# Performance work log

Measured on AMD Instinct MI355X. Metric: run time of the kernel, lower is better.

The kernel has to match this reference:

```python
import jax, jax.numpy as jnp
import numpy as np

B, R, K, D = 65536, 8, 8, 256


def setup_inputs() -> dict:
    key = jax.random.key(0)
    ks = jax.random.split(key, 7)
    return {
        "fine_memory": jax.random.normal(ks[0], (B, R, D), dtype=jnp.float32),
        "compressed_memory": jax.random.normal(ks[1], (B, K, D), dtype=jnp.float32),
        "fm_count": jax.random.randint(ks[2], (B,), 0, R + 1),
        "new_segment": jax.random.normal(ks[3], (B, D), dtype=jnp.float32),
        "valid_mask": jax.random.randint(ks[4], (B,), 0, 2).astype(bool),
        "conv_w": jax.random.normal(ks[5], (D, D, 2), dtype=jnp.float32) * 0.05,
        "conv_b": jax.random.normal(ks[6], (D,), dtype=jnp.float32) * 0.05,
    }


def reference(fine_memory, compressed_memory, fm_count, new_segment, valid_mask, conv_w, conv_b):
    """Vectorized CompressiveMemory.update().

    Per sample b (only where valid_mask[b]):
      - if fm_count[b] < R: write new_segment into fm slot fm_count[b]; count += 1
      - else: c_new = Conv1d([cm_last, fm_oldest]); shift cm left, append c_new;
              shift fm left, append new_segment.
    """
    b, r, d = fine_memory.shape
    insert = valid_mask & (fm_count < r)          # (B,) append into free slot
    shift = valid_mask & (fm_count >= r)          # (B,) FIFO shift + compress

    # --- insert branch: masked one-hot scatter of new_segment at position fm_count
    onehot = (jnp.arange(r)[None, :] == fm_count[:, None]) & insert[:, None]  # (B,R)
    fm_ins = jnp.where(onehot[:, :, None], new_segment[:, None, :], fine_memory)

    # --- shift branch: compress [cm_last, fm_oldest] with 2-tap conv (out,in,k)
    c_new = (jnp.einsum('bi,oi->bo', compressed_memory[:, -1], conv_w[:, :, 0])
             + jnp.einsum('bi,oi->bo', fine_memory[:, 0], conv_w[:, :, 1])
             + conv_b)  # (B,D)
    cm_shift = jnp.concatenate([compressed_memory[:, 1:], c_new[:, None, :]], axis=1)
    fm_shift = jnp.concatenate([fine_memory[:, 1:], new_segment[:, None, :]], axis=1)

    fm_new = jnp.where(shift[:, None, None], fm_shift, fm_ins)
    cm_new = jnp.where(shift[:, None, None], cm_shift, compressed_memory)
    fm_count_new = fm_count + insert.astype(fm_count.dtype)
    return fm_new, cm_new, fm_count_new
```

## Files before the change

### kernel.cpp

```cpp
#include <hip/hip_runtime.h>


#define NB 65536
#define RR 8
#define KK 8
#define DD 256
#define WFLOATS (DD * DD * 2)

typedef float f4 __attribute__((ext_vector_type(4)));

static __device__ __forceinline__ f4 ntload(const float* p) {
    return __builtin_nontemporal_load((const f4*)p);
}
static __device__ __forceinline__ void ntstore(float* p, f4 v) {
    __builtin_nontemporal_store(v, (f4*)p);
}

__global__ __launch_bounds__(256) void transpose_pack(
    const float* __restrict__ W, float* __restrict__ Wt2)
{
    int t = blockIdx.x * 256 + threadIdx.x;
    int o = t >> 9;
    int m = t & 511;
    Wt2[(size_t)(m >> 2) * (DD * 4) + o * 4 + (m & 3)] = W[t];
}

__global__ __launch_bounds__(256) void fused_update(
    const float* __restrict__ fm,
    const float* __restrict__ cm,
    const int* __restrict__ cnt_in,
    const float* __restrict__ seg,
    const int* __restrict__ valid,
    const float* __restrict__ Wt2,
    const float* __restrict__ bias,
    float* __restrict__ out_fm,
    float* __restrict__ out_cm,
    float* __restrict__ out_cnt)
{
    __shared__ float xbuf[512];

    const int b    = blockIdx.x;
    const int tid  = threadIdx.x;
    const int w    = tid >> 6;
    const int lane = tid & 63;
    const int c    = lane << 2;

    const int  cnt = cnt_in[b];
    const bool v   = valid[b] != 0;
    const bool ins = v && (cnt < RR);
    const bool shf = v && (cnt >= RR);

    const float* fmb  = fm  + (size_t)b * (RR * DD);
    const float* cmb  = cm  + (size_t)b * (KK * DD);
    const float* segb = seg + (size_t)b * DD;
    float* ofm = out_fm + (size_t)b * (RR * DD);
    float* ocm = out_cm + (size_t)b * (KK * DD);

    const int r0 = w, r1 = w + 4;

    const float* f0src = shf ? fmb + (r0 + 1) * DD
                             : (ins && r0 == cnt) ? segb : fmb + r0 * DD;
    const float* f1src = shf ? ((r1 < 7) ? fmb + (r1 + 1) * DD : segb)
                             : (ins && r1 == cnt) ? segb : fmb + r1 * DD;
    const bool   c1st  = !(shf && r1 == 7);
    const float* c0src = cmb + (shf ? r0 + 1 : r0) * DD;
    const float* c1src = c1st ? cmb + (shf ? r1 + 1 : r1) * DD : cmb;

    f4 a  = ntload(f0src + c);
    f4 bq = ntload(f1src + c);
    f4 d  = ntload(c0src + c);
    f4 e  = ntload(c1src + c);

    ntstore(ofm + r0 * DD + c, a);
    ntstore(ofm + r1 * DD + c, bq);
    ntstore(ocm + r0 * DD + c, d);
    if (c1st) ntstore(ocm + r1 * DD + c, e);

    if (tid == 0)
        out_cnt[b] = (float)(cnt + (ins ? 1 : 0));

    if (shf) {
        const float cv = cmb[(KK - 1) * DD + tid];
        const float fv = fmb[tid];
        xbuf[tid * 2]     = cv;
        xbuf[tid * 2 + 1] = fv;
        __syncthreads();

        float acc = 0.f;
        const float* wp = Wt2 + tid * 4;
        #pragma unroll 8
        for (int m4 = 0; m4 < 128; ++m4) {
            const f4 wq = *(const f4*)(wp + (size_t)m4 * (DD * 4));
            const f4 xq = *(const f4*)&xbuf[m4 * 4];
            acc += xq.x * wq.x + xq.y * wq.y + xq.z * wq.z + xq.w * wq.w;
        }
        acc += bias[tid];
        ocm[(KK - 1) * DD + tid] = acc;
    }
}

extern "C" void kernel_launch(void* const* d_in, const int* in_sizes, int n_in,
                              void* d_out, int out_size, void* d_ws, size_t ws_size,
                              hipStream_t stream) {
    const float* fm    = (const float*)d_in[0];
    const float* cm    = (const float*)d_in[1];
    const int*   cnt   = (const int*)d_in[2];
    const float* seg   = (const float*)d_in[3];
    const int*   valid = (const int*)d_in[4];
    const float* W     = (const float*)d_in[5];
    const float* bias  = (const float*)d_in[6];

    float* out_fm  = (float*)d_out;
    float* out_cm  = out_fm + (size_t)NB * RR * DD;
    float* out_cnt = out_cm + (size_t)NB * KK * DD;

    float* Wt2 = (float*)d_ws;

    hipLaunchKernelGGL(transpose_pack, dim3(WFLOATS / 256), dim3(256), 0, stream, W, Wt2);
    hipLaunchKernelGGL(fused_update, dim3(NB), dim3(256), 0, stream,
                       fm, cm, cnt, seg, valid, Wt2, bias, out_fm, out_cm, out_cnt);
}
```

Baseline: 417.4 us.

## Process eight samples per block in pairs with prefetched per-sample metadata

Each block now handles G=8 samples, processing two at a time so eight 16-byte loads are in flight per thread before the stores. The count and valid flags for the next pair are prefetched. The grid shrinks by 8x, which cuts block launch overhead. In exchange, each block serializes up to eight conv matvecs with extra barriers, and the smaller grid leaves less parallelism to hide memory latency.

```diff
diff --git a/kernel.cpp b/kernel.cpp
--- a/kernel.cpp
+++ b/kernel.cpp
@@ -6,6 +6,7 @@
 #define KK 8
 #define DD 256
 #define WFLOATS (DD * DD * 2)
+#define G 8
 
 typedef float f4 __attribute__((ext_vector_type(4)));
 
@@ -25,6 +26,27 @@
     Wt2[(size_t)(m >> 2) * (DD * 4) + o * 4 + (m & 3)] = W[t];
 }
 
+static __device__ __forceinline__ void conv_inline(
+    const float* __restrict__ cmb, const float* __restrict__ fmb,
+    const float* __restrict__ Wt2, const float* __restrict__ bias,
+    float* __restrict__ ocm, float* xbuf, int tid)
+{
+    xbuf[tid * 2]     = cmb[(KK - 1) * DD + tid];
+    xbuf[tid * 2 + 1] = fmb[tid];
+    __syncthreads();
+    float acc = 0.f;
+    const float* wp = Wt2 + tid * 4;
+    #pragma unroll 8
+    for (int m4 = 0; m4 < 128; ++m4) {
+        const f4 wq = *(const f4*)(wp + (size_t)m4 * (DD * 4));
+        const f4 xq = *(const f4*)&xbuf[m4 * 4];
+        acc += xq.x * wq.x + xq.y * wq.y + xq.z * wq.z + xq.w * wq.w;
+    }
+    acc += bias[tid];
+    ocm[(KK - 1) * DD + tid] = acc;
+    __syncthreads();
+}
+
 __global__ __launch_bounds__(256) void fused_update(
     const float* __restrict__ fm,
     const float* __restrict__ cm,
@@ -39,63 +61,81 @@
 {
     __shared__ float xbuf[512];
 
-    const int b    = blockIdx.x;
     const int tid  = threadIdx.x;
     const int w    = tid >> 6;
     const int lane = tid & 63;
     const int c    = lane << 2;
-
-    const int  cnt = cnt_in[b];
-    const bool v   = valid[b] != 0;
-    const bool ins = v && (cnt < RR);
-    const bool shf = v && (cnt >= RR);
-
-    const float* fmb  = fm  + (size_t)b * (RR * DD);
-    const float* cmb  = cm  + (size_t)b * (KK * DD);
-    const float* segb = seg + (size_t)b * DD;
-    float* ofm = out_fm + (size_t)b * (RR * DD);
-    float* ocm = out_cm + (size_t)b * (KK * DD);
+    const int base = blockIdx.x * G;
 
     const int r0 = w, r1 = w + 4;
 
-    const float* f0src = shf ? fmb + (r0 + 1) * DD
-                             : (ins && r0 == cnt) ? segb : fmb + r0 * DD;
-    const float* f1src = shf ? ((r1 < 7) ? fmb + (r1 + 1) * DD : segb)
-                             : (ins && r1 == cnt) ? segb : fmb + r1 * DD;
-    const bool   c1st  = !(shf && r1 == 7);
-    const float* c0src = cmb + (shf ? r0 + 1 : r0) * DD;
-    const float* c1src = c1st ? cmb + (shf ? r1 + 1 : r1) * DD : cmb;
+    int nxt_cA = cnt_in[base + 0], nxt_cB = cnt_in[base + 1];
+    int nxt_vA = valid[base + 0],  nxt_vB = valid[base + 1];
 
-    f4 a  = ntload(f0src + c);
-    f4 bq = ntload(f1src + c);
-    f4 d  = ntload(c0src + c);
-    f4 e  = ntload(c1src + c);
+    for (int j = 0; j < G; j += 2) {
+        const int bA = base + j, bB = base + j + 1;
+        const int cntA = nxt_cA, cntB = nxt_cB;
+        const bool vA = nxt_vA != 0, vB = nxt_vB != 0;
+        if (j + 2 < G) {
+            nxt_cA = cnt_in[bA + 2]; nxt_cB = cnt_in[bB + 2];
+            nxt_vA = valid[bA + 2];  nxt_vB = valid[bB + 2];
+        }
 
-    ntstore(ofm + r0 * DD + c, a);
-    ntstore(ofm + r1 * DD + c, bq);
-    ntstore(ocm + r0 * DD + c, d);
-    if (c1st) ntstore(ocm + r1 * DD + c, e);
+        const bool insA = vA && (cntA < RR), shfA = vA && (cntA >= RR);
+        const bool insB = vB && (cntB < RR), shfB = vB && (cntB >= RR);
 
-    if (tid == 0)
-        out_cnt[b] = (float)(cnt + (ins ? 1 : 0));
+        const float* fmA  = fm  + (size_t)bA * (RR * DD);
+        const float* cmA  = cm  + (size_t)bA * (KK * DD);
+        const float* segA = seg + (size_t)bA * DD;
+        const float* fmB  = fm  + (size_t)bB * (RR * DD);
+        const float* cmB  = cm  + (size_t)bB * (KK * DD);
+        const float* segB = seg + (size_t)bB * DD;
+        float* ofmA = out_fm + (size_t)bA * (RR * DD);
+        float* ocmA = out_cm + (size_t)bA * (KK * DD);
+        float* ofmB = out_fm + (size_t)bB * (RR * DD);
+        float* ocmB = out_cm + (size_t)bB * (KK * DD);
 
-    if (shf) {
-        const float cv = cmb[(KK - 1) * DD + tid];
-        const float fv = fmb[tid];
-        xbuf[tid * 2]     = cv;
-        xbuf[tid * 2 + 1] = fv;
-        __syncthreads();
+        const float* f0A = shfA ? fmA + (r0 + 1) * DD
+                                : (insA && r0 == cntA) ? segA : fmA + r0 * DD;
+        const float* f1A = shfA ? ((r1 < 7) ? fmA + (r1 + 1) * DD : segA)
+                                : (insA && r1 == cntA) ? segA : fmA + r1 * DD;
+        const bool   c1A = !(shfA && r1 == 7);
+        const float* c0A = cmA + (shfA ? r0 + 1 : r0) * DD;
+        const float* c1Ap = c1A ? cmA + (shfA ? r1 + 1 : r1) * DD : cmA;
 
-        float acc = 0.f;
-        const float* wp = Wt2 + tid * 4;
-        #pragma unroll 8
-        for (int m4 = 0; m4 < 128; ++m4) {
-            const f4 wq = *(const f4*)(wp + (size_t)m4 * (DD * 4));
-            const f4 xq = *(const f4*)&xbuf[m4 * 4];
-            acc += xq.x * wq.x + xq.y * wq.y + xq.z * wq.z + xq.w * wq.w;
+        const float* f0B = shfB ? fmB + (r0 + 1) * DD
+                                : (insB && r0 == cntB) ? segB : fmB + r0 * DD;
+        const float* f1B = shfB ? ((r1 < 7) ? fmB + (r1 + 1) * DD : segB)
+                                : (insB && r1 == cntB) ? segB : fmB + r1 * DD;
+        const bool   c1B = !(shfB && r1 == 7);
+        const float* c0B = cmB + (shfB ? r0 + 1 : r0) * DD;
+        const float* c1Bp = c1B ? cmB + (shfB ? r1 + 1 : r1) * DD : cmB;
+
+        f4 a0 = ntload(f0A + c);
+        f4 a1 = ntload(f1A + c);
+        f4 a2 = ntload(c0A + c);
+        f4 a3 = ntload(c1Ap + c);
+        f4 b0 = ntload(f0B + c);
+        f4 b1 = ntload(f1B + c);
+        f4 b2 = ntload(c0B + c);
+        f4 b3 = ntload(c1Bp + c);
+
+        ntstore(ofmA + r0 * DD + c, a0);
+        ntstore(ofmA + r1 * DD + c, a1);
+        ntstore(ocmA + r0 * DD + c, a2);
+        if (c1A) ntstore(ocmA + r1 * DD + c, a3);
+        ntstore(ofmB + r0 * DD + c, b0);
+        ntstore(ofmB + r1 * DD + c, b1);
+        ntstore(ocmB + r0 * DD + c, b2);
+        if (c1B) ntstore(ocmB + r1 * DD + c, b3);
+
+        if (tid == 0) {
+            out_cnt[bA] = (float)(cntA + (insA ? 1 : 0));
+            out_cnt[bB] = (float)(cntB + (insB ? 1 : 0));
         }
-        acc += bias[tid];
-        ocm[(KK - 1) * DD + tid] = acc;
+
+        if (shfA) conv_inline(cmA, fmA, Wt2, bias, ocmA, xbuf, tid);
+        if (shfB) conv_inline(cmB, fmB, Wt2, bias, ocmB, xbuf, tid);
     }
 }
 
@@ -117,6 +157,6 @@
     float* Wt2 = (float*)d_ws;
 
     hipLaunchKernelGGL(transpose_pack, dim3(WFLOATS / 256), dim3(256), 0, stream, W, Wt2);
-    hipLaunchKernelGGL(fused_update, dim3(NB), dim3(256), 0, stream,
+    hipLaunchKernelGGL(fused_update, dim3(NB / G), dim3(256), 0, stream,
                        fm, cm, cnt, seg, valid, Wt2, bias, out_fm, out_cm, out_cnt);
 }
```

New measurement: 446.0 us. 1.07x slower.
